# Optimization experiments

Measured on AMD Instinct MI355X. Metric: run time of the kernel, lower is better.

## Reference

```python
import jax, jax.numpy as jnp
import numpy as np

N, E = 10000, 320000
IN, HID, HEADS, OUT = 128, 32, 8, 64
NEG_SLOPE = 0.2  # PyG GATv2Conv default negative_slope


def _glorot(k, shape):
    fan = shape[0] + shape[-1]
    return jax.random.normal(k, shape, jnp.float32) * (2.0 / fan) ** 0.5


def setup_inputs() -> dict:
    key = jax.random.key(0)
    ks = jax.random.split(key, 12)
    D2 = HEADS * HID  # 256
    inp = {
        "x": jax.random.normal(ks[0], (N, IN), jnp.float32),
        "edge_index": jax.random.randint(ks[1], (2, E), 0, N, jnp.int32),
        # layer 1: IN -> HID per head, HEADS heads, concat
        "Wl1": _glorot(ks[2], (IN, D2)), "bl1": jnp.zeros((D2,), jnp.float32),
        "Wr1": _glorot(ks[3], (IN, D2)), "br1": jnp.zeros((D2,), jnp.float32),
        "att1": _glorot(ks[4], (HEADS, HID)), "bias1": jnp.zeros((D2,), jnp.float32),
        # layer 2: D2 -> HID per head, HEADS heads, concat
        "Wl2": _glorot(ks[5], (D2, D2)), "bl2": jnp.zeros((D2,), jnp.float32),
        "Wr2": _glorot(ks[6], (D2, D2)), "br2": jnp.zeros((D2,), jnp.float32),
        "att2": _glorot(ks[7], (HEADS, HID)), "bias2": jnp.zeros((D2,), jnp.float32),
        # layer 3: D2 -> OUT, 1 head
        "Wl3": _glorot(ks[8], (D2, OUT)), "bl3": jnp.zeros((OUT,), jnp.float32),
        "Wr3": _glorot(ks[9], (D2, OUT)), "br3": jnp.zeros((OUT,), jnp.float32),
        "att3": _glorot(ks[10], (1, OUT)), "bias3": jnp.zeros((OUT,), jnp.float32),
    }
    return inp


def _segment_softmax(scores, seg, n):
    # softmax over edges grouped by destination node
    m = jax.ops.segment_max(scores, seg, num_segments=n)
    m = jnp.where(jnp.isfinite(m), m, 0.0)  # guard isolated nodes
    ex = jnp.exp(scores - m[seg])
    denom = jax.ops.segment_sum(ex, seg, num_segments=n)
    return ex / (denom[seg] + 1e-16)


def _gatv2_conv(x, src, dst, Wl, bl, Wr, br, att, bias, heads, ch, n):
    gl = (x @ Wl + bl).reshape(n, heads, ch)  # source-side transform [N,H,C]
    gr = (x @ Wr + br).reshape(n, heads, ch)  # target-side transform [N,H,C]
    e = jax.nn.leaky_relu(gl[src] + gr[dst], NEG_SLOPE)  # [E,H,C]
    score = jnp.einsum('ehc,hc->eh', e, att)  # per-edge per-head attention logits
    alpha = _segment_softmax(score, dst, n)  # [E,H]; attention dropout p=0.6 is identity in eval
    out = jax.ops.segment_sum(alpha[:, :, None] * gl[src], dst, num_segments=n)  # [N,H,C]
    return out.reshape(n, heads * ch) + bias


def reference(x, edge_index, Wl1, bl1, Wr1, br1, att1, bias1,
              Wl2, bl2, Wr2, br2, att2, bias2,
              Wl3, bl3, Wr3, br3, att3, bias3):
    src, dst = edge_index[0], edge_index[1]
    n = x.shape[0]
    # F.dropout(p=0.6) layers are identity in eval mode
    h = jax.nn.elu(_gatv2_conv(x, src, dst, Wl1, bl1, Wr1, br1, att1, bias1, HEADS, HID, n))
    h = jax.nn.elu(_gatv2_conv(h, src, dst, Wl2, bl2, Wr2, br2, att2, bias2, HEADS, HID, n))
    h = _gatv2_conv(h, src, dst, Wl3, bl3, Wr3, br3, att3, bias3, 1, OUT, n)
    return jax.nn.sigmoid(h)
```

## Files before the change

kernel.cpp:

```cpp
#include <hip/hip_runtime.h>
#include <math.h>

#define N_NODES 10000
#define N_EDGES 320000
#define D_IN    128
#define D2      256
#define HEADS   8
#define HID     32
#define D_OUT   64

typedef _Float16 h2   __attribute__((ext_vector_type(2)));
typedef _Float16 f16x8 __attribute__((ext_vector_type(8)));
typedef float    f32x4 __attribute__((ext_vector_type(4)));

__device__ __forceinline__ float fdot2(h2 a, h2 b, float c) {
#if __has_builtin(__builtin_amdgcn_fdot2)
    return __builtin_amdgcn_fdot2(a, b, c, false);
#else
    return fmaf((float)a.x, (float)b.x, fmaf((float)a.y, (float)b.y, c));
#endif
}
__device__ __forceinline__ h2 bch2(unsigned u) { return __builtin_bit_cast(h2, u); }
__device__ __forceinline__ unsigned packf(float a, float b) {
    h2 h = {(_Float16)a, (_Float16)b};
    return __builtin_bit_cast(unsigned, h);
}

__global__ void zero_deg(int* __restrict__ deg) {
    const int i = blockIdx.x * 256 + threadIdx.x;
    if (i < N_NODES) deg[i] = 0;
}

__global__ void prep_all(const float* __restrict__ x, unsigned* __restrict__ xh,
                         const float* __restrict__ a1, unsigned* __restrict__ a1h,
                         const float* __restrict__ a2, unsigned* __restrict__ a2h,
                         const float* __restrict__ a3, unsigned* __restrict__ a3h,
                         const float* __restrict__ W1l, const float* __restrict__ W1r,
                         const float* __restrict__ W2l, const float* __restrict__ W2r,
                         const float* __restrict__ W3l, const float* __restrict__ W3r,
                         _Float16* __restrict__ T1l, _Float16* __restrict__ T1r,
                         _Float16* __restrict__ T2l, _Float16* __restrict__ T2r,
                         _Float16* __restrict__ T3l, _Float16* __restrict__ T3r,
                         const int* __restrict__ ei, int* __restrict__ deg) {
    const int b = blockIdx.x, t = threadIdx.x;
    if (b < 2500) {
        const int i = b * 256 + t;
        const float2 f = *reinterpret_cast<const float2*>(&x[2 * i]);
        xh[i] = packf(f.x, f.y);
    } else if (b == 2500) {
        if (t < 128) a1h[t] = packf(a1[2 * t], a1[2 * t + 1]);
    } else if (b == 2501) {
        if (t < 128) a2h[t] = packf(a2[2 * t], a2[2 * t + 1]);
    } else if (b == 2502) {
        if (t < 32) a3h[t] = packf(a3[2 * t], a3[2 * t + 1]);
    } else if (b < 2559) {
        __shared__ float tl[64][65];
        const int wb = b - 2503;
        const float* Wsrc; _Float16* Wdst; int K, M, tile;
        if (wb < 16)      { K = 128; M = 256; const bool r = wb >= 8;  Wsrc = r ? W1r : W1l; Wdst = r ? T1r : T1l; tile = wb & 7; }
        else if (wb < 48) { K = 256; M = 256; const bool r = wb >= 32; Wsrc = r ? W2r : W2l; Wdst = r ? T2r : T2l; tile = (wb - 16) & 15; }
        else              { K = 256; M = 64;  const bool r = wb >= 52; Wsrc = r ? W3r : W3l; Wdst = r ? T3r : T3l; tile = (wb - 48) & 3; }
        const int ktiles = K >> 6;
        const int k0 = (tile % ktiles) * 64, c0 = (tile / ktiles) * 64;
        const int rr = t >> 6, cc = t & 63;
        for (int i = 0; i < 64; i += 4)
            tl[i + rr][cc] = Wsrc[(size_t)(k0 + i + rr) * M + c0 + cc];
        __syncthreads();
        for (int i = 0; i < 64; i += 4)
            Wdst[(size_t)(c0 + i + rr) * K + k0 + cc] = (_Float16)tl[cc][i + rr];
    } else {
        const int e = (b - 2559) * 256 + t;
        if (e < N_EDGES) atomicAdd(&deg[ei[N_EDGES + e]], 1);
    }
}

template<int K, bool HOUT>
__global__ __launch_bounds__(256) void gemm_dual_mfma(
        const unsigned* __restrict__ Ah,
        const _Float16* __restrict__ Wtl, const float* __restrict__ bl,
        const _Float16* __restrict__ Wtr, const float* __restrict__ br,
        void* __restrict__ glv, void* __restrict__ grv,
        int Mtot, int nrows) {
    constexpr int AS = K + 8;
    __shared__ __align__(16) _Float16 Asm[64 * AS];
    __shared__ __align__(16) _Float16 Wsm[2][64 * 40];

    const int t = threadIdx.x;
    const int wave = t >> 6, lane = t & 63;
    const int lrow = lane & 15, lgrp = lane >> 4;
    const int row0 = blockIdx.x * 64, col0 = blockIdx.y * 64;

    {
        constexpr int CPR = K / 8;
        const int ar = t / CPR, ac = t % CPR;
        for (int i = 0; i < 64; i += 256 / CPR) {
            const int row = row0 + i + ar;
            uint4 v = make_uint4(0u, 0u, 0u, 0u);
            if (row < nrows) v = *reinterpret_cast<const uint4*>(&Ah[(size_t)row * (K / 2) + ac * 4]);
            *reinterpret_cast<uint4*>(&Asm[(i + ar) * AS + ac * 8]) = v;
        }
    }

    f32x4 accL[4], accR[4];
#pragma unroll
    for (int cf = 0; cf < 4; ++cf) { accL[cf] = (f32x4)0.0f; accR[cf] = (f32x4)0.0f; }

    const int wcol = t >> 2, wch = t & 3;

    for (int ks = 0; ks < K / 32; ++ks) {
        __syncthreads();
        {
            const uint4 vl = *reinterpret_cast<const uint4*>(&Wtl[(size_t)(col0 + wcol) * K + ks * 32 + wch * 8]);
            const uint4 vr = *reinterpret_cast<const uint4*>(&Wtr[(size_t)(col0 + wcol) * K + ks * 32 + wch * 8]);
            *reinterpret_cast<uint4*>(&Wsm[0][wcol * 40 + wch * 8]) = vl;
            *reinterpret_cast<uint4*>(&Wsm[1][wcol * 40 + wch * 8]) = vr;
        }
        __syncthreads();

        const f16x8 a = *reinterpret_cast<const f16x8*>(
            &Asm[(wave * 16 + lrow) * AS + ks * 32 + lgrp * 8]);
#pragma unroll
        for (int cf = 0; cf < 4; ++cf) {
            const f16x8 b_l = *reinterpret_cast<const f16x8*>(&Wsm[0][(cf * 16 + lrow) * 40 + lgrp * 8]);
            const f16x8 b_r = *reinterpret_cast<const f16x8*>(&Wsm[1][(cf * 16 + lrow) * 40 + lgrp * 8]);
            accL[cf] = __builtin_amdgcn_mfma_f32_16x16x32_f16(a, b_l, accL[cf], 0, 0, 0);
            accR[cf] = __builtin_amdgcn_mfma_f32_16x16x32_f16(a, b_r, accR[cf], 0, 0, 0);
        }
    }

#pragma unroll
    for (int cf = 0; cf < 4; ++cf) {
        const int col = col0 + cf * 16 + lrow;
        const float bll = bl[col], brr = br[col];
#pragma unroll
        for (int r = 0; r < 4; ++r) {
            const int row = row0 + wave * 16 + lgrp * 4 + r;
            if (row < nrows) {
                if constexpr (HOUT) {
                    _Float16* glh = (_Float16*)glv;
                    _Float16* grh = (_Float16*)grv;
                    glh[(size_t)row * Mtot + col] = (_Float16)(accL[cf][r] + bll);
                    grh[(size_t)row * Mtot + col] = (_Float16)(accR[cf][r] + brr);
                } else {
                    float* glf = (float*)glv;
                    float* grf = (float*)grv;
                    glf[(size_t)row * Mtot + col] = accL[cf][r] + bll;
                    grf[(size_t)row * Mtot + col] = accR[cf][r] + brr;
                }
            }
        }
    }
}

__global__ void scan_rowptr(const int* __restrict__ deg,
                            int* __restrict__ row_ptr, int* __restrict__ cursor) {
    __shared__ int part[1024];
    const int t = threadIdx.x;
    const int base = t * 10;
    int loc[10];
    int s = 0;
#pragma unroll
    for (int i = 0; i < 10; ++i) {
        const int v = (base + i < N_NODES) ? deg[base + i] : 0;
        loc[i] = s; s += v;
    }
    part[t] = s;
    __syncthreads();
    for (int d = 1; d < 1024; d <<= 1) {
        const int v = (t >= d) ? part[t - d] : 0;
        __syncthreads();
        part[t] += v;
        __syncthreads();
    }
    const int off = (t > 0) ? part[t - 1] : 0;
#pragma unroll
    for (int i = 0; i < 10; ++i) {
        const int idx = base + i;
        if (idx < N_NODES) {
            const int r = off + loc[i];
            row_ptr[idx] = r; cursor[idx] = r;
        }
    }
    if (t == 0) row_ptr[N_NODES] = N_EDGES;
}

__global__ void scatter_edges(const int* __restrict__ ei, int* __restrict__ cursor,
                              int* __restrict__ esrc) {
    const int e = blockIdx.x * blockDim.x + threadIdx.x;
    if (e < N_EDGES) {
        const int pos = atomicAdd(&cursor[ei[N_EDGES + e]], 1);
        esrc[pos] = ei[e];
    }
}

__global__ __launch_bounds__(256) void gat_wave_h2(
        const int* __restrict__ row_ptr, const int* __restrict__ esrc,
        const unsigned* __restrict__ gl, const unsigned* __restrict__ gr,
        const unsigned* __restrict__ atth, const float* __restrict__ bias,
        unsigned* __restrict__ hout) {
    constexpr int MU = D2 / 2;
    const int wid  = threadIdx.x >> 6;
    const int lane = threadIdx.x & 63;
    const int half = lane >> 5;
    const int sub  = lane & 31;
    const int n = blockIdx.x * 4 + wid;
    if (n >= N_NODES) return;
    const int u4 = sub * 4;
    const int c0 = sub * 8;

    h2 grn[4], av[4];
    {
        const uint4 u = *reinterpret_cast<const uint4*>(&gr[(size_t)n * MU + u4]);
        grn[0] = bch2(u.x); grn[1] = bch2(u.y); grn[2] = bch2(u.z); grn[3] = bch2(u.w);
        const uint4 a = *reinterpret_cast<const uint4*>(&atth[u4]);
        av[0] = bch2(a.x); av[1] = bch2(a.y); av[2] = bch2(a.z); av[3] = bch2(a.w);
    }
    const h2 hz = {(_Float16)0.f, (_Float16)0.f};
    const h2 hp = {(_Float16)0.2f, (_Float16)0.2f};

    float acc[8] = {0.f, 0.f, 0.f, 0.f, 0.f, 0.f, 0.f, 0.f};
    float denom = 0.0f;

    const int beg = row_ptr[n], end = row_ptr[n + 1];

    for (int base = beg; base < end; base += 64) {
        const int len = min(64, end - base);
        const int npairs = (len + 1) >> 1;
        const int myid = (base + lane < end) ? esrc[base + lane] : 0;

#define LOADP(k) (*reinterpret_cast<const uint4*>(&gl[(size_t)__shfl(myid, 2 * (k) + half) * MU + u4]))
        uint4 g0 = LOADP(0);
        uint4 g1 = (npairs > 1) ? LOADP(1) : g0;
        uint4 g2 = (npairs > 2) ? LOADP(2) : g0;
        uint4 g3 = (npairs > 3) ? LOADP(3) : g0;
        uint4 g4 = (npairs > 4) ? LOADP(4) : g0;
        uint4 g5 = (npairs > 5) ? LOADP(5) : g0;
        uint4 g6 = (npairs > 6) ? LOADP(6) : g0;
        uint4 g7 = (npairs > 7) ? LOADP(7) : g0;

        for (int i = 0; i < npairs; ++i) {
            const uint4 nxt = (i + 8 < npairs) ? LOADP(i + 8) : g0;

            const h2 G[4] = {bch2(g0.x), bch2(g0.y), bch2(g0.z), bch2(g0.w)};
            float s = 0.0f;
#pragma unroll
            for (int q = 0; q < 4; ++q) {
                const h2 v = G[q] + grn[q];
                const h2 lr = __builtin_elementwise_min(v, hz) * hp +
                              __builtin_elementwise_max(v, hz);
                s = fdot2(lr, av[q], s);
            }
            s += __shfl_xor(s, 1, 64);
            s += __shfl_xor(s, 2, 64);
            s = ((2 * i + half) < len) ? s : -INFINITY;

            const float e1 = __expf(s);
            denom += e1;
#pragma unroll
            for (int q = 0; q < 4; ++q) {
                acc[2 * q]     = fmaf(e1, (float)G[q].x, acc[2 * q]);
                acc[2 * q + 1] = fmaf(e1, (float)G[q].y, acc[2 * q + 1]);
            }
            g0 = g1; g1 = g2; g2 = g3; g3 = g4; g4 = g5; g5 = g6; g6 = g7; g7 = nxt;
        }
#undef LOADP
    }

    denom += __shfl_xor(denom, 32, 64);
#pragma unroll
    for (int v2 = 0; v2 < 8; ++v2) acc[v2] += __shfl_xor(acc[v2], 32, 64);

    if (half == 0) {
        const float inv = 1.0f / (denom + 1e-16f);
        const float4 b0 = *reinterpret_cast<const float4*>(&bias[c0]);
        const float4 b1 = *reinterpret_cast<const float4*>(&bias[c0 + 4]);
        const float bb[8] = {b0.x, b0.y, b0.z, b0.w, b1.x, b1.y, b1.z, b1.w};
        float r[8];
#pragma unroll
        for (int v2 = 0; v2 < 8; ++v2) {
            float val = acc[v2] * inv + bb[v2];
            r[v2] = val > 0.0f ? val : expm1f(val);
        }
        uint4 o;
        o.x = packf(r[0], r[1]); o.y = packf(r[2], r[3]);
        o.z = packf(r[4], r[5]); o.w = packf(r[6], r[7]);
        *reinterpret_cast<uint4*>(&hout[(size_t)n * MU + u4]) = o;
    }
}

__global__ __launch_bounds__(256) void gat_group3h(
        const int* __restrict__ row_ptr, const int* __restrict__ esrc,
        const unsigned* __restrict__ gl, const unsigned* __restrict__ gr,
        const unsigned* __restrict__ atth, const float* __restrict__ bias,
        float* __restrict__ out) {
    constexpr int MU = D_OUT / 2;
    const int wid  = threadIdx.x >> 6;
    const int lane = threadIdx.x & 63;
    const int g    = lane >> 4;
    const int sub  = lane & 15;
    const int n = blockIdx.x * 16 + wid * 4 + g;
    const bool nvalid = (n < N_NODES);
    const int u2 = sub * 2, c0 = sub * 4;

    h2 grn0, grn1, a0, a1;
    {
        const uint2 u = *reinterpret_cast<const uint2*>(&gr[(size_t)(nvalid ? n : 0) * MU + u2]);
        grn0 = bch2(u.x); grn1 = bch2(u.y);
        const uint2 au = *reinterpret_cast<const uint2*>(&atth[u2]);
        a0 = bch2(au.x); a1 = bch2(au.y);
    }
    const h2 hz = {(_Float16)0.f, (_Float16)0.f};
    const h2 hp = {(_Float16)0.2f, (_Float16)0.2f};

    float acc[4] = {0.f, 0.f, 0.f, 0.f};
    float denom = 0.0f;

    const int beg = nvalid ? row_ptr[n] : 0;
    const int deg = nvalid ? (row_ptr[n + 1] - beg) : 0;

    for (int off = 0; __any(off < deg); off += 16) {
        const int myid = (off + sub < deg) ? esrc[beg + off + sub] : 0;

#define GLD(j) (*reinterpret_cast<const uint2*>(&gl[(size_t)__shfl(myid, (g << 4) + (j)) * MU + u2]))
        uint2 r0 = GLD(0), r1 = GLD(1), r2 = GLD(2), r3 = GLD(3), r4 = GLD(4), r5 = GLD(5);
#pragma unroll
        for (int j = 0; j < 16; ++j) {
            const uint2 nxt = (j + 6 < 16) ? GLD(j + 6) : r0;
            const h2 G0 = bch2(r0.x), G1 = bch2(r0.y);
            const h2 v0 = G0 + grn0, v1 = G1 + grn1;
            const h2 lr0 = __builtin_elementwise_min(v0, hz) * hp + __builtin_elementwise_max(v0, hz);
            const h2 lr1 = __builtin_elementwise_min(v1, hz) * hp + __builtin_elementwise_max(v1, hz);
            float s = fdot2(lr1, a1, fdot2(lr0, a0, 0.0f));
            s += __shfl_xor(s, 1, 64);
            s += __shfl_xor(s, 2, 64);
            s += __shfl_xor(s, 4, 64);
            s += __shfl_xor(s, 8, 64);
            s = ((off + j) < deg) ? s : -INFINITY;

            const float e1 = __expf(s);
            denom += e1;
            acc[0] = fmaf(e1, (float)G0.x, acc[0]);
            acc[1] = fmaf(e1, (float)G0.y, acc[1]);
            acc[2] = fmaf(e1, (float)G1.x, acc[2]);
            acc[3] = fmaf(e1, (float)G1.y, acc[3]);
            r0 = r1; r1 = r2; r2 = r3; r3 = r4; r4 = r5; r5 = nxt;
        }
#undef GLD
    }

    if (nvalid) {
        const float inv = 1.0f / (denom + 1e-16f);
        const float4 b4 = *reinterpret_cast<const float4*>(&bias[c0]);
        float4 r;
        r.x = 1.0f / (1.0f + __expf(-(acc[0] * inv + b4.x)));
        r.y = 1.0f / (1.0f + __expf(-(acc[1] * inv + b4.y)));
        r.z = 1.0f / (1.0f + __expf(-(acc[2] * inv + b4.z)));
        r.w = 1.0f / (1.0f + __expf(-(acc[3] * inv + b4.w)));
        *reinterpret_cast<float4*>(&out[(size_t)n * D_OUT + c0]) = r;
    }
}

extern "C" void kernel_launch(void* const* d_in, const int* in_sizes, int n_in,
                              void* d_out, int out_size, void* d_ws, size_t ws_size,
                              hipStream_t stream) {
    const float* x    = (const float*)d_in[0];
    const int*   ei   = (const int*)  d_in[1];
    const float* Wl1  = (const float*)d_in[2];
    const float* bl1  = (const float*)d_in[3];
    const float* Wr1  = (const float*)d_in[4];
    const float* br1  = (const float*)d_in[5];
    const float* att1 = (const float*)d_in[6];
    const float* bi1  = (const float*)d_in[7];
    const float* Wl2  = (const float*)d_in[8];
    const float* bl2  = (const float*)d_in[9];
    const float* Wr2  = (const float*)d_in[10];
    const float* br2  = (const float*)d_in[11];
    const float* att2 = (const float*)d_in[12];
    const float* bi2  = (const float*)d_in[13];
    const float* Wl3  = (const float*)d_in[14];
    const float* bl3  = (const float*)d_in[15];
    const float* Wr3  = (const float*)d_in[16];
    const float* br3  = (const float*)d_in[17];
    const float* att3 = (const float*)d_in[18];
    const float* bi3  = (const float*)d_in[19];

    float* out = (float*)d_out;

    unsigned* ws   = (unsigned*)d_ws;
    unsigned* xh   = ws;
    unsigned* gl16 = xh   + (size_t)N_NODES * 64;
    unsigned* gr16 = gl16 + (size_t)N_NODES * 128;
    unsigned* h16  = gr16 + (size_t)N_NODES * 128;
    unsigned* gl3  = h16  + (size_t)N_NODES * 128;
    unsigned* gr3  = gl3  + (size_t)N_NODES * 32;
    _Float16* T1l  = (_Float16*)(gr3 + (size_t)N_NODES * 32);
    _Float16* T1r  = T1l + 32768;
    _Float16* T2l  = T1r + 32768;
    _Float16* T2r  = T2l + 65536;
    _Float16* T3l  = T2r + 65536;
    _Float16* T3r  = T3l + 16384;
    unsigned* ath1 = (unsigned*)(T3r + 16384);
    unsigned* ath2 = ath1 + 128;
    unsigned* ath3 = ath2 + 128;
    int* deg     = (int*)(ath3 + 32);
    int* row_ptr = deg + N_NODES;
    int* cursor  = row_ptr + N_NODES + 1;
    int* esrc    = cursor + N_NODES;

    zero_deg<<<(N_NODES + 255) / 256, 256, 0, stream>>>(deg);
    prep_all<<<2559 + (N_EDGES + 255) / 256, 256, 0, stream>>>(
        x, xh, att1, ath1, att2, ath2, att3, ath3,
        Wl1, Wr1, Wl2, Wr2, Wl3, Wr3,
        T1l, T1r, T2l, T2r, T3l, T3r,
        ei, deg);
    scan_rowptr<<<1, 1024, 0, stream>>>(deg, row_ptr, cursor);
    scatter_edges<<<(N_EDGES + 255) / 256, 256, 0, stream>>>(ei, cursor, esrc);

    const int RT64 = (N_NODES + 63) / 64;

    gemm_dual_mfma<D_IN, true><<<dim3(RT64, 4), 256, 0, stream>>>(
        xh, T1l, bl1, T1r, br1, gl16, gr16, D2, N_NODES);
    gat_wave_h2<<<(N_NODES + 3) / 4, 256, 0, stream>>>(
        row_ptr, esrc, gl16, gr16, ath1, bi1, h16);

    gemm_dual_mfma<D2, true><<<dim3(RT64, 4), 256, 0, stream>>>(
        h16, T2l, bl2, T2r, br2, gl16, gr16, D2, N_NODES);
    gat_wave_h2<<<(N_NODES + 3) / 4, 256, 0, stream>>>(
        row_ptr, esrc, gl16, gr16, ath2, bi2, h16);

    gemm_dual_mfma<D2, true><<<dim3(RT64, 1), 256, 0, stream>>>(
        h16, T3l, bl3, T3r, br3, gl3, gr3, D_OUT, N_NODES);
    gat_group3h<<<(N_NODES + 15) / 16, 256, 0, stream>>>(
        row_ptr, esrc, gl3, gr3, ath3, bi3, out);
}
```

Measured before the change: 183.0 us.

## Replace rolling register prefetch with fully unrolled double-banked gather batches

Swaps the rolling 8-deep register queue for two unrolled banks of 8 gathered rows. One bank is loaded while the other is processed, covering up to 32 pairs (64 edges) per chunk. This removes the per-iteration register shifting and the loop-carried conditional load, and lets the compiler schedule batched independent loads. In exchange the code is bigger, register pressure is higher, and edges past the last loaded bank are processed in groups of 8 with masking, which wastes work on tails.

After: 184.9 us. Within noise of the previous version (+1.0%).

```diff
diff --git a/kernel.cpp b/kernel.cpp
--- a/kernel.cpp
+++ b/kernel.cpp
@@ -229,41 +229,56 @@
         const int myid = (base + lane < end) ? esrc[base + lane] : 0;
 
 #define LOADP(k) (*reinterpret_cast<const uint4*>(&gl[(size_t)__shfl(myid, 2 * (k) + half) * MU + u4]))
-        uint4 g0 = LOADP(0);
-        uint4 g1 = (npairs > 1) ? LOADP(1) : g0;
-        uint4 g2 = (npairs > 2) ? LOADP(2) : g0;
-        uint4 g3 = (npairs > 3) ? LOADP(3) : g0;
-        uint4 g4 = (npairs > 4) ? LOADP(4) : g0;
-        uint4 g5 = (npairs > 5) ? LOADP(5) : g0;
-        uint4 g6 = (npairs > 6) ? LOADP(6) : g0;
-        uint4 g7 = (npairs > 7) ? LOADP(7) : g0;
-
-        for (int i = 0; i < npairs; ++i) {
-            const uint4 nxt = (i + 8 < npairs) ? LOADP(i + 8) : g0;
-
-            const h2 G[4] = {bch2(g0.x), bch2(g0.y), bch2(g0.z), bch2(g0.w)};
-            float s = 0.0f;
-#pragma unroll
-            for (int q = 0; q < 4; ++q) {
-                const h2 v = G[q] + grn[q];
-                const h2 lr = __builtin_elementwise_min(v, hz) * hp +
-                              __builtin_elementwise_max(v, hz);
-                s = fdot2(lr, av[q], s);
+#define LOADG(BANK, BASE)                                     \
+        _Pragma("unroll")                                     \
+        for (int p = 0; p < 8; ++p) BANK[p] = LOADP((BASE) + p);
+#define PROCG(BANK, BASE)                                                          \
+        _Pragma("unroll")                                                          \
+        for (int p = 0; p < 8; ++p) {                                              \
+            const h2 G0 = bch2(BANK[p].x), G1 = bch2(BANK[p].y);                   \
+            const h2 G2 = bch2(BANK[p].z), G3 = bch2(BANK[p].w);                   \
+            const h2 v0 = G0 + grn[0], v1 = G1 + grn[1];                           \
+            const h2 v2 = G2 + grn[2], v3 = G3 + grn[3];                           \
+            float s = 0.0f;                                                        \
+            s = fdot2(__builtin_elementwise_min(v0, hz) * hp +                     \
+                      __builtin_elementwise_max(v0, hz), av[0], s);                \
+            s = fdot2(__builtin_elementwise_min(v1, hz) * hp +                     \
+                      __builtin_elementwise_max(v1, hz), av[1], s);                \
+            s = fdot2(__builtin_elementwise_min(v2, hz) * hp +                     \
+                      __builtin_elementwise_max(v2, hz), av[2], s);                \
+            s = fdot2(__builtin_elementwise_min(v3, hz) * hp +                     \
+                      __builtin_elementwise_max(v3, hz), av[3], s);                \
+            s += __shfl_xor(s, 1, 64);                                             \
+            s += __shfl_xor(s, 2, 64);                                             \
+            s = ((2 * ((BASE) + p) + half) < len) ? s : -INFINITY;                 \
+            const float e1 = __expf(s);                                            \
+            denom += e1;                                                           \
+            acc[0] = fmaf(e1, (float)G0.x, acc[0]);                                \
+            acc[1] = fmaf(e1, (float)G0.y, acc[1]);                                \
+            acc[2] = fmaf(e1, (float)G1.x, acc[2]);                                \
+            acc[3] = fmaf(e1, (float)G1.y, acc[3]);                                \
+            acc[4] = fmaf(e1, (float)G2.x, acc[4]);                                \
+            acc[5] = fmaf(e1, (float)G2.y, acc[5]);                                \
+            acc[6] = fmaf(e1, (float)G3.x, acc[6]);                                \
+            acc[7] = fmaf(e1, (float)G3.y, acc[7]);                                \
+        }
+
+        uint4 A[8], B[8];
+        LOADG(A, 0);
+        if (npairs > 8)  { LOADG(B, 8); }
+        PROCG(A, 0);
+        if (npairs > 8) {
+            if (npairs > 16) { LOADG(A, 16); }
+            PROCG(B, 8);
+            if (npairs > 16) {
+                if (npairs > 24) { LOADG(B, 24); }
+                PROCG(A, 16);
+                if (npairs > 24) { PROCG(B, 24); }
             }
-            s += __shfl_xor(s, 1, 64);
-            s += __shfl_xor(s, 2, 64);
-            s = ((2 * i + half) < len) ? s : -INFINITY;
-
-            const float e1 = __expf(s);
-            denom += e1;
-#pragma unroll
-            for (int q = 0; q < 4; ++q) {
-                acc[2 * q]     = fmaf(e1, (float)G[q].x, acc[2 * q]);
-                acc[2 * q + 1] = fmaf(e1, (float)G[q].y, acc[2 * q + 1]);
-            }
-            g0 = g1; g1 = g2; g2 = g3; g3 = g4; g4 = g5; g5 = g6; g6 = g7; g7 = nxt;
         }
 #undef LOADP
+#undef LOADG
+#undef PROCG
     }
 
     denom += __shfl_xor(denom, 32, 64);
```
